# Kernel tuning notes

Hardware: AMD Instinct MI355X
Metric: run time of the kernel (lower is better)

## Reference

```python
import jax, jax.numpy as jnp
import numpy as np

HEADS = 16
NUM_CHUNKS = 8  # min(int(log2(4096))+1, 8)


def setup_inputs() -> dict:
    key = jax.random.key(0)
    ks = jax.random.split(key, 6)
    B, T, C = 4, 4096, 1024
    s = 1.0 / np.sqrt(C)
    x = jax.random.normal(ks[0], (B, T, C), jnp.float32)
    Wqkv = jax.random.normal(ks[1], (3 * C, C), jnp.float32) * s
    Wout = jax.random.normal(ks[2], (C, C), jnp.float32) * s
    bout = jnp.zeros((C,), jnp.float32)
    Wl1 = jax.random.normal(ks[3], (64, 1), jnp.float32)
    bl1 = jnp.zeros((64,), jnp.float32)
    Wl2 = jax.random.normal(ks[4], (HEADS, 64), jnp.float32) * 0.125
    bl2 = jnp.zeros((HEADS,), jnp.float32)
    return dict(x=x, Wqkv=Wqkv, Wout=Wout, bout=bout, Wl1=Wl1, bl1=bl1, Wl2=Wl2, bl2=bl2)


def reference(x, Wqkv, Wout, bout, Wl1, bl1, Wl2, bl2):
    B, T, C = x.shape
    H = HEADS
    dh = C // H
    nc = NUM_CHUNKS
    cs = T // nc
    scale = dh ** (-0.5)

    # qkv projection (torch Linear: x @ W.T), split, to [B,H,T,dh]
    qkv = x @ Wqkv.T  # [B,T,3C]
    q, k, v = jnp.split(qkv, 3, axis=-1)
    def heads(t):
        return t.reshape(B, T, H, dh).transpose(0, 2, 1, 3)
    q, k, v = heads(q), heads(k), heads(v)

    # lambda gates from log positions: [T,1] -> [T,H] -> [H,T]
    log_pos = jnp.log(jnp.arange(T, dtype=jnp.float32) + 1.0)[:, None]
    h1 = jax.nn.relu(log_pos @ Wl1.T + bl1)            # [T,64]
    lam = jax.nn.sigmoid(h1 @ Wl2.T + bl2).T           # [H,T]
    lam = lam.reshape(H, nc, cs)                        # per-chunk key gates

    # block-local (chunked) attention, fully vectorized over chunks
    qc = q.reshape(B, H, nc, cs, dh)
    kc = k.reshape(B, H, nc, cs, dh)
    vc = v.reshape(B, H, nc, cs, dh)
    scores = jnp.einsum('bhnqd,bhnkd->bhnqk', qc, kc) * scale
    scores = scores * lam[None, :, :, None, :]          # gate keys pre-softmax
    attn = jax.nn.softmax(scores, axis=-1)
    out = jnp.einsum('bhnqk,bhnkd->bhnqd', attn, vc)    # [B,H,nc,cs,dh]

    out = out.reshape(B, H, T, dh).transpose(0, 2, 1, 3).reshape(B, T, C)
    return out @ Wout.T + bout
```

## Files before the change

kernel.cpp:

```cpp
#include <hip/hip_runtime.h>
#include <hip/hip_bf16.h>

typedef unsigned short u16;
typedef __attribute__((ext_vector_type(8))) short v8s;
typedef __attribute__((ext_vector_type(4))) float v4f;
typedef __attribute__((ext_vector_type(4))) unsigned v4u;

#define DEV __device__ __forceinline__

DEV u16 f2bf(float f) {
  union { float f; unsigned u; } v; v.f = f;
  unsigned r = v.u + 0x7fffu + ((v.u >> 16) & 1u);
  return (u16)(r >> 16);
}

DEV unsigned pk2bf(float a, float b) {
  float2 t; t.x = a; t.y = b;
  __hip_bfloat162 p = __float22bfloat162_rn(t);
  union { __hip_bfloat162 h; unsigned u; } c; c.h = p;
  return c.u;
}

DEV void gload_lds16(const void* g, void* l) {
  __builtin_amdgcn_global_load_lds(
      (const __attribute__((address_space(1))) void*)g,
      (__attribute__((address_space(3))) void*)l, 16, 0, 0);
}

__global__ __launch_bounds__(256) void cvt_bf16(const float* __restrict__ in,
                                                u16* __restrict__ out, int n4) {
  int i = blockIdx.x * 256 + threadIdx.x;
  if (i >= n4) return;
  float4 v = ((const float4*)in)[i];
  ushort4 o;
  o.x = f2bf(v.x); o.y = f2bf(v.y); o.z = f2bf(v.z); o.w = f2bf(v.w);
  ((ushort4*)out)[i] = o;
}

__global__ __launch_bounds__(256) void lam_kernel(const float* __restrict__ Wl1,
    const float* __restrict__ bl1, const float* __restrict__ Wl2,
    const float* __restrict__ bl2, float* __restrict__ lam) {
  int t = blockIdx.x * 256 + threadIdx.x;
  float lp = logf((float)t + 1.0f);
  float h1[64];
#pragma unroll
  for (int j = 0; j < 64; ++j) h1[j] = fmaxf(lp * Wl1[j] + bl1[j], 0.0f);
#pragma unroll 1
  for (int h = 0; h < 16; ++h) {
    float z = bl2[h];
#pragma unroll
    for (int j = 0; j < 64; ++j) z += h1[j] * Wl2[h * 64 + j];
    lam[h * 4096 + t] = 0.125f / (1.0f + expf(-z));
  }
}

template <int MH>
DEV void mfma32(v4f (&acc)[8][4], const v8s (&a)[4][2], const v8s (&b)[4][2]) {
#pragma unroll
  for (int kk = 0; kk < 2; ++kk)
#pragma unroll
    for (int i = 0; i < 4; ++i)
#pragma unroll
      for (int j = 0; j < 4; ++j)
        acc[MH * 4 + i][j] = __builtin_amdgcn_mfma_f32_16x16x32_bf16(
            a[i][kk], b[j][kk], acc[MH * 4 + i][j], 0, 0, 0);
}

DEV void ldA(v8s (&a)[4][2], const u16* Ab, int wr, int mh, int lane) {
  const int l15 = lane & 15, g = lane >> 4;
#pragma unroll
  for (int i = 0; i < 4; ++i) {
    const int row = wr * 128 + mh * 64 + i * 16 + l15;
#pragma unroll
    for (int kk = 0; kk < 2; ++kk)
      a[i][kk] = *(const v8s*)(Ab + row * 64 + (((kk * 4 + g) ^ (row & 7)) << 3));
  }
}

DEV void ldB4(v8s (&b)[4][2], const u16* Bb, int wc, int lane) {
  const int l15 = lane & 15, g = lane >> 4;
#pragma unroll
  for (int j = 0; j < 4; ++j) {
    const int row = (j >> 1) * 128 + wc * 32 + (j & 1) * 16 + l15;
#pragma unroll
    for (int kk = 0; kk < 2; ++kk)
      b[j][kk] = *(const v8s*)(Bb + row * 64 + (((kk * 4 + g) ^ (row & 7)) << 3));
  }
}

template <int OUTF32>
__global__ __launch_bounds__(512, 2) void gemm256(const u16* __restrict__ A,
    const u16* __restrict__ Bt, void* __restrict__ Cout,
    const float* __restrict__ bias, int M, int N, int K) {
  __shared__ u16 As[2][256 * 64];
  __shared__ u16 Bs[2][256 * 64];
  const int tid = threadIdx.x;
  const int lane = tid & 63;
  const int nbn = N >> 8;
  const int nwg = gridDim.x;
  int wg = blockIdx.x;
  wg = (wg & 7) * (nwg >> 3) + (wg >> 3);
  const int m0 = (wg / nbn) << 8;
  const int n0 = (wg % nbn) << 8;
  const int wid = tid >> 6;
  const int wr = wid >> 2;
  const int wc = wid & 3;
  const int nkt = K >> 6;
  const int nit = nkt >> 1;

  auto SAu = [&](int buf, int kt, int u) {
    const int ur = tid >> 3;
    const int slot = (tid & 7) ^ (ur & 7);
    gload_lds16(A + (size_t)(m0 + u * 64 + ur) * K + kt * 64 + slot * 8,
                &As[buf][u * 4096 + (tid & ~63) * 8]);
  };
  auto SBu = [&](int buf, int kt, int u) {
    const int q = tid >> 3;
    const int grow = (((u & 1) * 2 + (q >> 5)) << 6) + ((u >> 1) << 5) + (q & 31);
    const int slot = (tid & 7) ^ (q & 7);
    gload_lds16(Bt + (size_t)(n0 + grow) * K + kt * 64 + slot * 8,
                &Bs[buf][u * 4096 + (tid & ~63) * 8]);
  };
  auto SA_ = [&](int buf, int kt, int mh) { SAu(buf, kt, mh); SAu(buf, kt, 2 + mh); };
  auto SB_ = [&](int buf, int kt, int nh) { SBu(buf, kt, nh * 2); SBu(buf, kt, nh * 2 + 1); };

  v4f acc[8][4] = {};
  v8s a[4][2], b[4][2];

  SA_(0, 0, 0); SA_(0, 0, 1); SB_(0, 0, 0); SB_(0, 0, 1);
  SA_(1, 1, 0); SB_(1, 1, 0); SB_(1, 1, 1);
  asm volatile("s_waitcnt vmcnt(6)" ::: "memory");
  asm volatile("s_barrier" ::: "memory");

#define PHASE(MHc, VM, ...)                                 \
  do { __VA_ARGS__; } while (0);                            \
  __builtin_amdgcn_s_setprio(1);                            \
  mfma32<MHc>(acc, a, b);                                   \
  __builtin_amdgcn_s_setprio(0);                            \
  if (VM) asm volatile("s_waitcnt vmcnt(6)" ::: "memory");  \
  asm volatile("s_barrier" ::: "memory");

  for (int it = 0; it < nit; ++it) {
    const int t0 = 2 * it;
    const int t1 = t0 + 1;
    const int t2 = (t0 + 2 < nkt) ? t0 + 2 : nkt - 1;
    const int t3 = (t0 + 3 < nkt) ? t0 + 3 : nkt - 1;
    ldA(a, As[0], wr, 0, lane); ldB4(b, Bs[0], wc, lane);
    PHASE(0, 0, SAu(1, t1, 1); SAu(1, t1, 3));
    ldA(a, As[0], wr, 1, lane);
    PHASE(1, 1, SB_(0, t2, 0); SB_(0, t2, 1); SAu(0, t2, 0); SAu(0, t2, 2));
    ldA(a, As[1], wr, 0, lane); ldB4(b, Bs[1], wc, lane);
    PHASE(0, 0, SAu(0, t2, 1); SAu(0, t2, 3));
    ldA(a, As[1], wr, 1, lane);
    PHASE(1, 1, SB_(1, t3, 0); SB_(1, t3, 1); SAu(1, t3, 0); SAu(1, t3, 2));
  }
#undef PHASE

  const int l15 = lane & 15, g4 = (lane >> 4) * 4;
#pragma unroll
  for (int i = 0; i < 8; ++i) {
#pragma unroll
    for (int j = 0; j < 4; ++j) {
      const int gr = m0 + wr * 128 + i * 16 + g4;
      const int gc = n0 + wc * 64 + j * 16 + l15;
      float bv = OUTF32 ? bias[gc] : 0.0f;
#pragma unroll
      for (int r = 0; r < 4; ++r) {
        float val = acc[i][j][r];
        if (OUTF32) ((float*)Cout)[(size_t)(gr + r) * N + gc] = val + bv;
        else ((u16*)Cout)[(size_t)(gr + r) * N + gc] = f2bf(val);
      }
    }
  }
}

__global__ __launch_bounds__(512, 2) void attn_chunk(const u16* __restrict__ qkv,
    const float* __restrict__ lam, u16* __restrict__ aout) {
  __shared__ u16 Ksm[512 * 64];
  __shared__ u16 Vt[64 * 520];
  __shared__ float lam_s[512];

  const int tid = threadIdx.x;
  const int lane = tid & 63;
  const int wid = tid >> 6;
  const int blk = blockIdx.x;
  const int c = blk & 7;
  const int h = (blk >> 3) & 15;
  const int b = blk >> 7;
  const size_t tok0 = (size_t)b * 4096 + c * 512;
  const u16* qb = qkv + tok0 * 3072 + h * 64;
  const u16* kb = qb + 1024;
  const u16* vb = qb + 2048;

  lam_s[tid] = lam[h * 4096 + c * 512 + tid];

#pragma unroll
  for (int i = 0; i < 8; ++i) {
    const int r = i * 64 + wid * 8 + (lane >> 3);
    const int f = (r & 3) | (((r >> 3) & 1) << 2);
    gload_lds16(kb + (size_t)r * 3072 + (((lane & 7) ^ f) << 3),
                &Ksm[(i * 64 + wid * 8) * 64]);
  }
  {
    const int pr = tid & 255;
    const int db0 = (tid >> 8) * 4;
#pragma unroll
    for (int dbi = 0; dbi < 4; ++dbi) {
      const int d0 = (db0 + dbi) * 8;
      v8s v0 = *(const v8s*)(vb + (size_t)(2 * pr) * 3072 + d0);
      v8s v1 = *(const v8s*)(vb + (size_t)(2 * pr + 1) * 3072 + d0);
#pragma unroll
      for (int j = 0; j < 8; ++j) {
        unsigned pk = (unsigned)(u16)v0[j] | ((unsigned)(u16)v1[j] << 16);
        *(unsigned*)&Vt[(d0 + j) * 520 + 2 * pr] = pk;
      }
    }
  }
  __syncthreads();

  const int l15 = lane & 15;
  const int gg = lane >> 4;
  const int rbase = ((l15 >> 2) << 3) + (l15 & 3);
  const int fsl = (l15 & 3) | (((l15 >> 2) & 1) << 2);
  const int sl0 = ((gg ^ fsl) << 3);
  const int sl1 = (((4 + gg) ^ fsl) << 3);

#pragma unroll 1
  for (int pass = 0; pass < 4; ++pass) {
    const int q0 = pass * 128 + wid * 16;
    const v8s qf0 = *(const v8s*)(qb + (size_t)(q0 + l15) * 3072 + gg * 8);
    const v8s qf1 = *(const v8s*)(qb + (size_t)(q0 + l15) * 3072 + 32 + gg * 8);

    float m = -1e30f, sum = 0.0f;
    v4f o[4] = {};

#pragma unroll 1
    for (int qtr = 0; qtr < 4; ++qtr) {
      v4f s[8];
#pragma unroll
      for (int kpl = 0; kpl < 4; ++kpl) {
#pragma unroll
        for (int hh = 0; hh < 2; ++hh) {
          const int rw = (qtr * 128 + kpl * 32 + rbase + hh * 4) << 6;
          v4f z = {0.f, 0.f, 0.f, 0.f};
          z = __builtin_amdgcn_mfma_f32_16x16x32_bf16(
              *(const v8s*)&Ksm[rw + sl0], qf0, z, 0, 0, 0);
          z = __builtin_amdgcn_mfma_f32_16x16x32_bf16(
              *(const v8s*)&Ksm[rw + sl1], qf1, z, 0, 0, 0);
          const v4f lv = *(const v4f*)&lam_s[qtr * 128 + kpl * 32 + gg * 8 + hh * 4];
          s[kpl * 2 + hh] = z * lv;
        }
      }
      v4f vm = s[0];
#pragma unroll
      for (int kt = 1; kt < 8; ++kt)
#pragma unroll
        for (int r = 0; r < 4; ++r) vm[r] = fmaxf(vm[r], s[kt][r]);
      float qmax = fmaxf(fmaxf(vm[0], vm[1]), fmaxf(vm[2], vm[3]));
      qmax = fmaxf(qmax, __shfl_xor(qmax, 16));
      qmax = fmaxf(qmax, __shfl_xor(qmax, 32));
      const float newm = fmaxf(m, qmax);
      const float scale = __expf(m - newm);
      m = newm;
      float psum = 0.f;
#pragma unroll
      for (int kt = 0; kt < 8; ++kt)
#pragma unroll
        for (int r = 0; r < 4; ++r) {
          s[kt][r] = __expf(s[kt][r] - m);
          psum += s[kt][r];
        }
      sum = sum * scale + psum;
#pragma unroll
      for (int dt = 0; dt < 4; ++dt)
#pragma unroll
        for (int r = 0; r < 4; ++r) o[dt][r] *= scale;

#pragma unroll
      for (int kpl = 0; kpl < 4; ++kpl) {
        v4u pwv;
        pwv.x = pk2bf(s[2 * kpl][0], s[2 * kpl][1]);
        pwv.y = pk2bf(s[2 * kpl][2], s[2 * kpl][3]);
        pwv.z = pk2bf(s[2 * kpl + 1][0], s[2 * kpl + 1][1]);
        pwv.w = pk2bf(s[2 * kpl + 1][2], s[2 * kpl + 1][3]);
        const v8s pf = __builtin_bit_cast(v8s, pwv);
#pragma unroll
        for (int dt = 0; dt < 4; ++dt) {
          const v8s vf = *(const v8s*)&Vt[(dt * 16 + l15) * 520 +
                                          (qtr * 4 + kpl) * 32 + gg * 8];
          o[dt] = __builtin_amdgcn_mfma_f32_16x16x32_bf16(vf, pf, o[dt], 0, 0, 0);
        }
      }
    }

    sum += __shfl_xor(sum, 16);
    sum += __shfl_xor(sum, 32);
    const float sminv = 1.0f / sum;

    const size_t obase = (tok0 + q0 + l15) * 1024 + h * 64;
#pragma unroll
    for (int dt = 0; dt < 4; ++dt) {
      ushort4 w;
      w.x = f2bf(o[dt][0] * sminv); w.y = f2bf(o[dt][1] * sminv);
      w.z = f2bf(o[dt][2] * sminv); w.w = f2bf(o[dt][3] * sminv);
      *(ushort4*)&aout[obase + dt * 16 + gg * 4] = w;
    }
  }
}

extern "C" void kernel_launch(void* const* d_in, const int* in_sizes, int n_in,
                              void* d_out, int out_size, void* d_ws, size_t ws_size,
                              hipStream_t stream) {
  const float* x    = (const float*)d_in[0];
  const float* Wqkv = (const float*)d_in[1];
  const float* Wout = (const float*)d_in[2];
  const float* bout = (const float*)d_in[3];
  const float* Wl1  = (const float*)d_in[4];
  const float* bl1  = (const float*)d_in[5];
  const float* Wl2  = (const float*)d_in[6];
  const float* bl2  = (const float*)d_in[7];
  float* out = (float*)d_out;

  char* ws = (char*)d_ws;
  u16* xbf    = (u16*)ws; ws += (size_t)16384 * 1024 * 2;
  u16* wqkvbf = (u16*)ws; ws += (size_t)3072 * 1024 * 2;
  u16* woutbf = (u16*)ws; ws += (size_t)1024 * 1024 * 2;
  u16* qkvbf  = (u16*)ws; ws += (size_t)16384 * 3072 * 2;
  u16* aoutbf = (u16*)ws; ws += (size_t)16384 * 1024 * 2;
  float* lam  = (float*)ws; ws += (size_t)16 * 4096 * 4;

  cvt_bf16<<<16384, 256, 0, stream>>>(x, xbf, 16777216 / 4);
  cvt_bf16<<<3072, 256, 0, stream>>>(Wqkv, wqkvbf, 3145728 / 4);
  cvt_bf16<<<1024, 256, 0, stream>>>(Wout, woutbf, 1048576 / 4);
  lam_kernel<<<16, 256, 0, stream>>>(Wl1, bl1, Wl2, bl2, lam);

  gemm256<0><<<dim3((16384 / 256) * (3072 / 256)), 512, 0, stream>>>(
      xbf, wqkvbf, qkvbf, nullptr, 16384, 3072, 1024);

  attn_chunk<<<512, 512, 0, stream>>>(qkvbf, lam, aoutbf);

  gemm256<1><<<dim3((16384 / 256) * (1024 / 256)), 512, 0, stream>>>(
      aoutbf, woutbf, out, bout, 16384, 1024, 1024);
}
```

Measured before the change: 255.7 us.

## Switch chunk attention to 32x32x16 MFMA tiles with lazy softmax rescaling

Rewrites the attention inner loop to use 32x32x16 bf16 MFMA tiles. Each wave now handles 32 queries per pass and steps through 32-key tiles. The V transpose in LDS is permuted so P can be fed straight from the accumulator layout. The online softmax skips rescaling unless the running max grows by more than a threshold, and launch bounds drop the minimum-blocks hint. The aim is fewer MFMA issues, LDS reads and shuffles per unit of work, at the cost of higher register pressure and possibly lower occupancy.

```diff
diff --git a/kernel.cpp b/kernel.cpp
--- a/kernel.cpp
+++ b/kernel.cpp
@@ -4,6 +4,7 @@
 typedef unsigned short u16;
 typedef __attribute__((ext_vector_type(8))) short v8s;
 typedef __attribute__((ext_vector_type(4))) float v4f;
+typedef __attribute__((ext_vector_type(16))) float v16f;
 typedef __attribute__((ext_vector_type(4))) unsigned v4u;
 
 #define DEV __device__ __forceinline__
@@ -174,7 +175,7 @@
   }
 }
 
-__global__ __launch_bounds__(512, 2) void attn_chunk(const u16* __restrict__ qkv,
+__global__ __launch_bounds__(512) void attn_chunk(const u16* __restrict__ qkv,
     const float* __restrict__ lam, u16* __restrict__ aout) {
   __shared__ u16 Ksm[512 * 64];
   __shared__ u16 Vt[64 * 520];
@@ -185,14 +186,14 @@
   const int wid = tid >> 6;
   const int blk = blockIdx.x;
   const int c = blk & 7;
-  const int h = (blk >> 3) & 15;
+  const int hd = (blk >> 3) & 15;
   const int b = blk >> 7;
   const size_t tok0 = (size_t)b * 4096 + c * 512;
-  const u16* qb = qkv + tok0 * 3072 + h * 64;
+  const u16* qb = qkv + tok0 * 3072 + hd * 64;
   const u16* kb = qb + 1024;
   const u16* vb = qb + 2048;
 
-  lam_s[tid] = lam[h * 4096 + c * 512 + tid];
+  lam_s[tid] = lam[hd * 4096 + c * 512 + tid];
 
 #pragma unroll
   for (int i = 0; i < 8; ++i) {
@@ -203,107 +204,101 @@
   }
   {
     const int pr = tid & 255;
+    const int k0 = 2 * pr;
+    const int kg = k0 & 31;
+    const int col = (k0 & ~31) + (kg & 16) + (((kg >> 2) & 1) << 3) +
+                    ((kg & 3) | ((kg & 8) >> 1));
     const int db0 = (tid >> 8) * 4;
 #pragma unroll
     for (int dbi = 0; dbi < 4; ++dbi) {
       const int d0 = (db0 + dbi) * 8;
-      v8s v0 = *(const v8s*)(vb + (size_t)(2 * pr) * 3072 + d0);
-      v8s v1 = *(const v8s*)(vb + (size_t)(2 * pr + 1) * 3072 + d0);
+      v8s v0 = *(const v8s*)(vb + (size_t)k0 * 3072 + d0);
+      v8s v1 = *(const v8s*)(vb + (size_t)(k0 + 1) * 3072 + d0);
 #pragma unroll
       for (int j = 0; j < 8; ++j) {
         unsigned pk = (unsigned)(u16)v0[j] | ((unsigned)(u16)v1[j] << 16);
-        *(unsigned*)&Vt[(d0 + j) * 520 + 2 * pr] = pk;
+        *(unsigned*)&Vt[(d0 + j) * 520 + col] = pk;
       }
     }
   }
   __syncthreads();
 
-  const int l15 = lane & 15;
-  const int gg = lane >> 4;
-  const int rbase = ((l15 >> 2) << 3) + (l15 & 3);
-  const int fsl = (l15 & 3) | (((l15 >> 2) & 1) << 2);
-  const int sl0 = ((gg ^ fsl) << 3);
-  const int sl1 = (((4 + gg) ^ fsl) << 3);
+  const int l31 = lane & 31;
+  const int hf = lane >> 5;
+  const int fk = (l31 & 3) | (((l31 >> 3) & 1) << 2);
 
 #pragma unroll 1
-  for (int pass = 0; pass < 4; ++pass) {
-    const int q0 = pass * 128 + wid * 16;
-    const v8s qf0 = *(const v8s*)(qb + (size_t)(q0 + l15) * 3072 + gg * 8);
-    const v8s qf1 = *(const v8s*)(qb + (size_t)(q0 + l15) * 3072 + 32 + gg * 8);
+  for (int pass = 0; pass < 2; ++pass) {
+    const int q0 = pass * 256 + wid * 32;
+    v8s qv[4];
+#pragma unroll
+    for (int dsec = 0; dsec < 4; ++dsec)
+      qv[dsec] = *(const v8s*)(qb + (size_t)(q0 + l31) * 3072 + dsec * 16 + hf * 8);
 
     float m = -1e30f, sum = 0.0f;
-    v4f o[4] = {};
+    v16f o0 = {}, o1 = {};
 
 #pragma unroll 1
-    for (int qtr = 0; qtr < 4; ++qtr) {
-      v4f s[8];
-#pragma unroll
-      for (int kpl = 0; kpl < 4; ++kpl) {
-#pragma unroll
-        for (int hh = 0; hh < 2; ++hh) {
-          const int rw = (qtr * 128 + kpl * 32 + rbase + hh * 4) << 6;
-          v4f z = {0.f, 0.f, 0.f, 0.f};
-          z = __builtin_amdgcn_mfma_f32_16x16x32_bf16(
-              *(const v8s*)&Ksm[rw + sl0], qf0, z, 0, 0, 0);
-          z = __builtin_amdgcn_mfma_f32_16x16x32_bf16(
-              *(const v8s*)&Ksm[rw + sl1], qf1, z, 0, 0, 0);
-          const v4f lv = *(const v4f*)&lam_s[qtr * 128 + kpl * 32 + gg * 8 + hh * 4];
-          s[kpl * 2 + hh] = z * lv;
-        }
-      }
-      v4f vm = s[0];
-#pragma unroll
-      for (int kt = 1; kt < 8; ++kt)
-#pragma unroll
-        for (int r = 0; r < 4; ++r) vm[r] = fmaxf(vm[r], s[kt][r]);
-      float qmax = fmaxf(fmaxf(vm[0], vm[1]), fmaxf(vm[2], vm[3]));
-      qmax = fmaxf(qmax, __shfl_xor(qmax, 16));
-      qmax = fmaxf(qmax, __shfl_xor(qmax, 32));
-      const float newm = fmaxf(m, qmax);
-      const float scale = __expf(m - newm);
-      m = newm;
-      float psum = 0.f;
-#pragma unroll
-      for (int kt = 0; kt < 8; ++kt)
-#pragma unroll
-        for (int r = 0; r < 4; ++r) {
-          s[kt][r] = __expf(s[kt][r] - m);
-          psum += s[kt][r];
-        }
-      sum = sum * scale + psum;
-#pragma unroll
-      for (int dt = 0; dt < 4; ++dt)
-#pragma unroll
-        for (int r = 0; r < 4; ++r) o[dt][r] *= scale;
-
-#pragma unroll
-      for (int kpl = 0; kpl < 4; ++kpl) {
-        v4u pwv;
-        pwv.x = pk2bf(s[2 * kpl][0], s[2 * kpl][1]);
-        pwv.y = pk2bf(s[2 * kpl][2], s[2 * kpl][3]);
-        pwv.z = pk2bf(s[2 * kpl + 1][0], s[2 * kpl + 1][1]);
-        pwv.w = pk2bf(s[2 * kpl + 1][2], s[2 * kpl + 1][3]);
-        const v8s pf = __builtin_bit_cast(v8s, pwv);
-#pragma unroll
-        for (int dt = 0; dt < 4; ++dt) {
-          const v8s vf = *(const v8s*)&Vt[(dt * 16 + l15) * 520 +
-                                          (qtr * 4 + kpl) * 32 + gg * 8];
-          o[dt] = __builtin_amdgcn_mfma_f32_16x16x32_bf16(vf, pf, o[dt], 0, 0, 0);
-        }
-      }
+    for (int kt = 0; kt < 16; ++kt) {
+      v16f acc = {};
+#pragma unroll
+      for (int dsec = 0; dsec < 4; ++dsec) {
+        const v8s kf = *(const v8s*)&Ksm[(kt * 32 + l31) * 64 +
+                                         (((dsec * 2 + hf) ^ fk) << 3)];
+        acc = __builtin_amdgcn_mfma_f32_32x32x16_bf16(kf, qv[dsec], acc, 0, 0, 0);
+      }
+#pragma unroll
+      for (int a = 0; a < 4; ++a) {
+        const v4f lv = *(const v4f*)&lam_s[kt * 32 + a * 8 + hf * 4];
+#pragma unroll
+        for (int i = 0; i < 4; ++i) acc[4 * a + i] *= lv[i];
+      }
+      float tm = acc[0];
+#pragma unroll
+      for (int r = 1; r < 16; ++r) tm = fmaxf(tm, acc[r]);
+      tm = fmaxf(tm, __shfl_xor(tm, 32));
+      if (!__all(tm <= m + 8.0f)) {
+        const float nm = fmaxf(m, tm);
+        const float sc = __expf(m - nm);
+        sum *= sc;
+        o0 *= sc; o1 *= sc;
+        m = nm;
+      }
+      float ps = 0.0f;
+#pragma unroll
+      for (int r = 0; r < 16; ++r) { acc[r] = __expf(acc[r] - m); ps += acc[r]; }
+      sum += ps;
+      v4u pa, pb;
+      pa.x = pk2bf(acc[0], acc[1]);   pa.y = pk2bf(acc[2], acc[3]);
+      pa.z = pk2bf(acc[4], acc[5]);   pa.w = pk2bf(acc[6], acc[7]);
+      pb.x = pk2bf(acc[8], acc[9]);   pb.y = pk2bf(acc[10], acc[11]);
+      pb.z = pk2bf(acc[12], acc[13]); pb.w = pk2bf(acc[14], acc[15]);
+      const v8s pfA = __builtin_bit_cast(v8s, pa);
+      const v8s pfB = __builtin_bit_cast(v8s, pb);
+      const int vcol = kt * 32 + hf * 8;
+      const v8s vA0 = *(const v8s*)&Vt[l31 * 520 + vcol];
+      const v8s vB0 = *(const v8s*)&Vt[l31 * 520 + vcol + 16];
+      const v8s vA1 = *(const v8s*)&Vt[(32 + l31) * 520 + vcol];
+      const v8s vB1 = *(const v8s*)&Vt[(32 + l31) * 520 + vcol + 16];
+      o0 = __builtin_amdgcn_mfma_f32_32x32x16_bf16(vA0, pfA, o0, 0, 0, 0);
+      o0 = __builtin_amdgcn_mfma_f32_32x32x16_bf16(vB0, pfB, o0, 0, 0, 0);
+      o1 = __builtin_amdgcn_mfma_f32_32x32x16_bf16(vA1, pfA, o1, 0, 0, 0);
+      o1 = __builtin_amdgcn_mfma_f32_32x32x16_bf16(vB1, pfB, o1, 0, 0, 0);
     }
 
-    sum += __shfl_xor(sum, 16);
     sum += __shfl_xor(sum, 32);
-    const float sminv = 1.0f / sum;
-
-    const size_t obase = (tok0 + q0 + l15) * 1024 + h * 64;
-#pragma unroll
-    for (int dt = 0; dt < 4; ++dt) {
-      ushort4 w;
-      w.x = f2bf(o[dt][0] * sminv); w.y = f2bf(o[dt][1] * sminv);
-      w.z = f2bf(o[dt][2] * sminv); w.w = f2bf(o[dt][3] * sminv);
-      *(ushort4*)&aout[obase + dt * 16 + gg * 4] = w;
+    const float sv = 1.0f / sum;
+
+    const size_t obase = (tok0 + q0 + l31) * 1024 + hd * 64;
+#pragma unroll
+    for (int a = 0; a < 4; ++a) {
+      ushort4 w0, w1;
+      w0.x = f2bf(o0[4 * a + 0] * sv); w0.y = f2bf(o0[4 * a + 1] * sv);
+      w0.z = f2bf(o0[4 * a + 2] * sv); w0.w = f2bf(o0[4 * a + 3] * sv);
+      w1.x = f2bf(o1[4 * a + 0] * sv); w1.y = f2bf(o1[4 * a + 1] * sv);
+      w1.z = f2bf(o1[4 * a + 2] * sv); w1.w = f2bf(o1[4 * a + 3] * sv);
+      *(ushort4*)&aout[obase + 8 * a + 4 * hf] = w0;
+      *(ushort4*)&aout[obase + 32 + 8 * a + 4 * hf] = w1;
     }
   }
 }
```

Measured after the change: 248.4 us. 1.03x faster.
